# Performance work log

Hardware: AMD Instinct MI355X
Metric: run time of the kernel (lower is better)

Reference implementation:

```python
import jax, jax.numpy as jnp
import numpy as np

D_MODEL = 2048
DOWN = 512
UP = 1024
NUM_HEADS = 16
ROPE_DIM = 64
BS = 16
SEQ = 512
BASE = 10000.0
HEAD_DIM = D_MODEL // NUM_HEADS          # 128 (used only in the softmax scale)
V_HEAD_DIM = UP // NUM_HEADS             # 64


def _linear(x, W, b):
    # torch nn.Linear: y = x @ W.T + b, W shape (out, in)
    return x @ W.T + b


def _rope(x, num_heads, rope_dim):
    # Faithful to source RotaryEmbedding, including the swapped sin/cos caches:
    #   cos_pos = sin(pos*theta), sin_pos = cos(pos*theta)
    bs, L, _ = x.shape
    q = x.reshape(bs, L, num_heads, rope_dim).transpose(0, 2, 1, 3)  # (bs,h,L,d)
    theta = 1.0 / (BASE ** (jnp.arange(0, rope_dim, 2, dtype=jnp.float32) / rope_dim))
    ang = jnp.arange(L, dtype=jnp.float32)[:, None] * theta[None, :]   # (L, d/2)
    cos_pos = jnp.repeat(jnp.sin(ang), 2, axis=-1)  # (L, d) -- source quirk
    sin_pos = jnp.repeat(jnp.cos(ang), 2, axis=-1)
    q2 = jnp.stack([-q[..., 1::2], q[..., ::2]], axis=-1).reshape(bs, num_heads, L, rope_dim)
    return q * cos_pos + q2 * sin_pos


def setup_inputs() -> dict:
    key = jax.random.key(0)
    ks = jax.random.split(key, 18)
    s = 0.02
    d = {
        "h": jax.random.normal(ks[0], (BS, SEQ, D_MODEL), jnp.float32),
        "W_down_kv": jax.random.normal(ks[1], (DOWN, D_MODEL), jnp.float32) * s,
        "b_down_kv": jnp.zeros((DOWN,), jnp.float32),
        "W_up_k": jax.random.normal(ks[2], (UP, DOWN), jnp.float32) * s,
        "b_up_k": jnp.zeros((UP,), jnp.float32),
        "W_up_v": jax.random.normal(ks[3], (UP, DOWN), jnp.float32) * s,
        "b_up_v": jnp.zeros((UP,), jnp.float32),
        "W_down_q": jax.random.normal(ks[4], (DOWN, D_MODEL), jnp.float32) * s,
        "b_down_q": jnp.zeros((DOWN,), jnp.float32),
        "W_up_q": jax.random.normal(ks[5], (UP, DOWN), jnp.float32) * s,
        "b_up_q": jnp.zeros((UP,), jnp.float32),
        "W_qr": jax.random.normal(ks[6], (ROPE_DIM * NUM_HEADS, DOWN), jnp.float32) * s,
        "b_qr": jnp.zeros((ROPE_DIM * NUM_HEADS,), jnp.float32),
        "W_kr": jax.random.normal(ks[7], (ROPE_DIM, D_MODEL), jnp.float32) * s,
        "b_kr": jnp.zeros((ROPE_DIM,), jnp.float32),
        "W_fc": jax.random.normal(ks[8], (D_MODEL, NUM_HEADS * V_HEAD_DIM), jnp.float32) * s,
        "b_fc": jnp.zeros((D_MODEL,), jnp.float32),
    }
    return d


def reference(h, W_down_kv, b_down_kv, W_up_k, b_up_k, W_up_v, b_up_v,
              W_down_q, b_down_q, W_up_q, b_up_q, W_qr, b_qr,
              W_kr, b_kr, W_fc, b_fc):
    bs, L, _ = h.shape
    # low-rank KV path
    c_kv = _linear(h, W_down_kv, b_down_kv)             # (bs,L,down)
    k_c = _linear(c_kv, W_up_k, b_up_k)                 # (bs,L,up)
    v_c = _linear(c_kv, W_up_v, b_up_v)                 # (bs,L,up)
    # low-rank Q path
    c_q = _linear(h, W_down_q, b_down_q)                # (bs,L,down)
    q_c = _linear(c_q, W_up_q, b_up_q)                  # (bs,L,up)
    # rope (decoupled) path
    q_r = _rope(_linear(c_q, W_qr, b_qr), NUM_HEADS, ROPE_DIM)  # (bs,H,L,rope)
    k_r = _rope(_linear(h, W_kr, b_kr), 1, ROPE_DIM)            # (bs,1,L,rope)

    q_c = q_c.reshape(bs, L, NUM_HEADS, -1).transpose(0, 2, 1, 3)  # (bs,H,L,64)
    q = jnp.concatenate([q_c, q_r], axis=-1)                        # (bs,H,L,128)
    k_c = k_c.reshape(bs, L, NUM_HEADS, -1).transpose(0, 2, 1, 3)
    k_r = jnp.broadcast_to(k_r, (bs, NUM_HEADS, L, ROPE_DIM))       # shared across heads
    k = jnp.concatenate([k_c, k_r], axis=-1)

    scale = 1.0 / jnp.sqrt(jnp.float32(HEAD_DIM + ROPE_DIM))  # sqrt(192), per source
    scores = jnp.einsum('bhqd,bhkd->bhqk', q, k) * scale
    attn = jax.nn.softmax(scores, axis=-1)  # dropout is identity in eval mode

    v = v_c.reshape(bs, L, NUM_HEADS, V_HEAD_DIM).transpose(0, 2, 1, 3)
    out = jnp.einsum('bhqk,bhkd->bhqd', attn, v)
    out = out.transpose(0, 2, 1, 3).reshape(bs, L, -1)   # (bs,L,H*v_head_dim)
    return _linear(out, W_fc, b_fc)                      # (bs,L,d_model)
```

## Files before the change

kernel.cpp:

```cpp
#include <hip/hip_runtime.h>
#include <hip/hip_bf16.h>

typedef __bf16 bf16x8 __attribute__((ext_vector_type(8)));
typedef float f32x4 __attribute__((ext_vector_type(4)));
using u16 = unsigned short;
using u32 = unsigned int;

__device__ __forceinline__ float bf2f(u16 v) {
    unsigned int u = (unsigned int)v << 16;
    float f; __builtin_memcpy(&f, &u, 4); return f;
}
__device__ __forceinline__ u16 f2bf(float f) {
    unsigned int u; __builtin_memcpy(&u, &f, 4);
    u += 0x7FFFu + ((u >> 16) & 1u);
    return (u16)(u >> 16);
}

struct Cvt9 {
    const float* src[9];
    u16* dst[9];
    int end[9];
};
__global__ __launch_bounds__(256) void cvt_all(Cvt9 d, int total)
{
    int c = blockIdx.x * 256 + threadIdx.x;
    if (c >= total) return;
    int seg = 0;
    while (c >= d.end[seg]) ++seg;
    int local = c - (seg ? d.end[seg - 1] : 0);
    const float* s = d.src[seg] + (size_t)local * 8;
    float4 f0 = *(const float4*)s;
    float4 f1 = *(const float4*)(s + 4);
    u16 tmp[8] = { f2bf(f0.x), f2bf(f0.y), f2bf(f0.z), f2bf(f0.w),
                   f2bf(f1.x), f2bf(f1.y), f2bf(f1.z), f2bf(f1.w) };
    *(uint4*)(d.dst[seg] + (size_t)local * 8) = *(const uint4*)tmp;
}

struct Cpy7 {
    const float* src[7];
    float* dst[7];
    int end[7];
};
__global__ __launch_bounds__(256) void copy_f32(Cpy7 d, int total)
{
    int c = blockIdx.x * 256 + threadIdx.x;
    if (c >= total) return;
    int seg = 0;
    while (c >= d.end[seg]) ++seg;
    int local = c - (seg ? d.end[seg - 1] : 0);
    d.dst[seg][local] = d.src[seg][local];
}

template<bool CF>
__global__ __launch_bounds__(256) void gemm_v3(
    const u16* __restrict__ A0, const u16* __restrict__ B0, void* __restrict__ C0, const float* __restrict__ e0,
    const u16* __restrict__ A1, const u16* __restrict__ B1, void* __restrict__ C1, const float* __restrict__ e1,
    int ysplit, int lda, int ldb, int ldc, int N, int K)
{
    __shared__ __align__(16) u16 As[128 * 32];
    __shared__ __align__(16) u16 Bs[128 * 32];

    const int t = threadIdx.x;
    const int lane = t & 63;
    const int w = t >> 6;
    const int wm = w >> 1, wn = w & 1;
    const int l16 = lane & 15, quad = lane >> 4;
    const int m0 = blockIdx.x * 128;

    const u16* A; const u16* B; void* Cv; const float* bias; int yl;
    if ((int)blockIdx.y < ysplit) { A = A0; B = B0; Cv = C0; bias = e0; yl = blockIdx.y; }
    else                          { A = A1; B = B1; Cv = C1; bias = e1; yl = blockIdx.y - ysplit; }
    const int n0 = yl * 128;

    const int sub  = lane >> 2;
    const int slot = lane & 3;
    const int agc  = slot ^ ((sub >> 1) & 3);
    const int sfr  = (l16 >> 1) & 3;

    f32x4 acc[4][4];
#pragma unroll
    for (int i = 0; i < 4; ++i)
#pragma unroll
        for (int j = 0; j < 4; ++j) acc[i][j] = (f32x4){0.f, 0.f, 0.f, 0.f};

    for (int k0 = 0; k0 < K; k0 += 32) {
        __syncthreads();
#pragma unroll
        for (int c = 0; c < 2; ++c) {
            const int rr = w * 32 + c * 16;
            const u16* ga = A + (size_t)(m0 + rr + sub) * lda + k0 + agc * 8;
            __builtin_amdgcn_global_load_lds(
                (const __attribute__((address_space(1))) u32*)ga,
                (__attribute__((address_space(3))) u32*)&As[rr * 32], 16, 0, 0);
            const u16* gb = B + (size_t)(n0 + rr + sub) * ldb + k0 + agc * 8;
            __builtin_amdgcn_global_load_lds(
                (const __attribute__((address_space(1))) u32*)gb,
                (__attribute__((address_space(3))) u32*)&Bs[rr * 32], 16, 0, 0);
        }
        __syncthreads();

        bf16x8 af[4], bfr[4];
#pragma unroll
        for (int i = 0; i < 4; ++i)
            af[i] = *(const bf16x8*)&As[(wm * 64 + i * 16 + l16) * 32 + (quad ^ sfr) * 8];
#pragma unroll
        for (int j = 0; j < 4; ++j)
            bfr[j] = *(const bf16x8*)&Bs[(wn * 64 + j * 16 + l16) * 32 + (quad ^ sfr) * 8];
#pragma unroll
        for (int i = 0; i < 4; ++i)
#pragma unroll
            for (int j = 0; j < 4; ++j)
                acc[i][j] = __builtin_amdgcn_mfma_f32_16x16x32_bf16(af[i], bfr[j], acc[i][j], 0, 0, 0);
    }

#pragma unroll
    for (int j = 0; j < 4; ++j) {
        int col = n0 + wn * 64 + j * 16 + l16;
        if (col >= N) continue;
        float bv = bias[col];
#pragma unroll
        for (int i = 0; i < 4; ++i) {
#pragma unroll
            for (int r = 0; r < 4; ++r) {
                int row = m0 + wm * 64 + i * 16 + quad * 4 + r;
                float v = acc[i][j][r] + bv;
                if (CF) ((float*)Cv)[(size_t)row * ldc + col] = v;
                else    ((u16*)Cv)[(size_t)row * ldc + col] = f2bf(v);
            }
        }
    }
}

__global__ void rope_inplace(u16* __restrict__ buf, int ld, int col0, int ppr, int total)
{
    int idx = blockIdx.x * 256 + threadIdx.x;
    if (idx >= total) return;
    int row = idx / ppr;
    int pi  = idx - row * ppr;
    int grp = pi >> 5;
    int i   = pi & 31;
    int pos = row & 511;
    float theta = __expf(-(float)i * 0.2878231366242558f);
    float ang = (float)pos * theta;
    float s = sinf(ang), c = cosf(ang);
    size_t base = (size_t)row * ld + col0 + grp * 64 + 2 * i;
    float x0 = bf2f(buf[base]);
    float x1 = bf2f(buf[base + 1]);
    buf[base]     = f2bf(x0 * s - x1 * c);
    buf[base + 1] = f2bf(x1 * s + x0 * c);
}

__global__ __launch_bounds__(256) void attn_kernel(
    const u16* __restrict__ q_src,
    const u16* __restrict__ kv_src,
    const u16* __restrict__ kr_src,
    u16* __restrict__ o_dst, int ldo)
{
    __shared__ __align__(16) u16 Qs[64 * 136];
    __shared__ __align__(16) u16 Ks[64 * 136];
    __shared__ __align__(16) u16 Vt[64 * 72];
    __shared__ __align__(16) u16 Ps[64 * 72];

    const int t = threadIdx.x;
    const int lane = t & 63;
    const int w = t >> 6;
    const int l16 = lane & 15, quad = lane >> 4;
    const int qt = blockIdx.x;
    const int h  = blockIdx.y;
    const int b  = blockIdx.z;
    const int qrow0 = b * 512 + qt * 64;

#pragma unroll
    for (int p = 0; p < 4; ++p) {
        int ch = t + 256 * p;
        int r = ch >> 4;
        int col = (ch & 15) * 8;
        const u16* src = (col < 64)
            ? q_src + (size_t)(qrow0 + r) * 2048 + h * 64 + col
            : q_src + (size_t)(qrow0 + r) * 2048 + 1024 + h * 64 + (col - 64);
        *(uint4*)&Qs[r * 136 + col] = *(const uint4*)src;
    }

    float m_run[4], l_run[4];
    f32x4 o[4];
#pragma unroll
    for (int r = 0; r < 4; ++r) { m_run[r] = -1e30f; l_run[r] = 0.f; }
#pragma unroll
    for (int n = 0; n < 4; ++n) o[n] = (f32x4){0.f, 0.f, 0.f, 0.f};

    const float scale = 0.07216878364870323f;

    for (int kt = 0; kt < 8; ++kt) {
        __syncthreads();
        const int krow0 = b * 512 + kt * 64;
#pragma unroll
        for (int p = 0; p < 4; ++p) {
            int ch = t + 256 * p;
            int r = ch >> 4;
            int col = (ch & 15) * 8;
            const u16* src = (col < 64)
                ? kv_src + (size_t)(krow0 + r) * 2048 + h * 64 + col
                : kr_src + (size_t)(krow0 + r) * 1088 + 1024 + (col - 64);
            *(uint4*)&Ks[r * 136 + col] = *(const uint4*)src;
        }
#pragma unroll
        for (int p = 0; p < 2; ++p) {
            int ch = t + 256 * p;
            int r = ch >> 3;
            int v0 = (ch & 7) * 8;
            uint4 vv = *(const uint4*)(kv_src + (size_t)(krow0 + r) * 2048 + 1024 + h * 64 + v0);
            u16 tmp[8];
            __builtin_memcpy(tmp, &vv, 16);
#pragma unroll
            for (int j2 = 0; j2 < 8; ++j2)
                Vt[(v0 + j2) * 72 + r] = tmp[j2];
        }
        __syncthreads();

        f32x4 s[4];
#pragma unroll
        for (int n = 0; n < 4; ++n) s[n] = (f32x4){0.f, 0.f, 0.f, 0.f};
#pragma unroll
        for (int ks = 0; ks < 4; ++ks) {
            bf16x8 aq = *(const bf16x8*)&Qs[(w * 16 + l16) * 136 + ks * 32 + quad * 8];
#pragma unroll
            for (int n = 0; n < 4; ++n) {
                bf16x8 bk = *(const bf16x8*)&Ks[(n * 16 + l16) * 136 + ks * 32 + quad * 8];
                s[n] = __builtin_amdgcn_mfma_f32_16x16x32_bf16(aq, bk, s[n], 0, 0, 0);
            }
        }

        float mx[4], alpha[4], rs[4];
#pragma unroll
        for (int r = 0; r < 4; ++r) {
#pragma unroll
            for (int n = 0; n < 4; ++n) s[n][r] *= scale;
            mx[r] = fmaxf(fmaxf(s[0][r], s[1][r]), fmaxf(s[2][r], s[3][r]));
        }
#pragma unroll
        for (int d = 1; d < 16; d <<= 1)
#pragma unroll
            for (int r = 0; r < 4; ++r)
                mx[r] = fmaxf(mx[r], __shfl_xor(mx[r], d));
#pragma unroll
        for (int r = 0; r < 4; ++r) {
            float mnew = fmaxf(m_run[r], mx[r]);
            alpha[r] = __expf(m_run[r] - mnew);
            m_run[r] = mnew;
            rs[r] = 0.f;
#pragma unroll
            for (int n = 0; n < 4; ++n) {
                float pv = __expf(s[n][r] - mnew);
                s[n][r] = pv;
                rs[r] += pv;
            }
        }
#pragma unroll
        for (int d = 1; d < 16; d <<= 1)
#pragma unroll
            for (int r = 0; r < 4; ++r)
                rs[r] += __shfl_xor(rs[r], d);
#pragma unroll
        for (int r = 0; r < 4; ++r) {
            l_run[r] = l_run[r] * alpha[r] + rs[r];
#pragma unroll
            for (int n = 0; n < 4; ++n) o[n][r] *= alpha[r];
        }

#pragma unroll
        for (int n = 0; n < 4; ++n)
#pragma unroll
            for (int r = 0; r < 4; ++r)
                Ps[(w * 16 + quad * 4 + r) * 72 + n * 16 + l16] = f2bf(s[n][r]);
        __syncthreads();

#pragma unroll
        for (int kk = 0; kk < 2; ++kk) {
            bf16x8 ap = *(const bf16x8*)&Ps[(w * 16 + l16) * 72 + kk * 32 + quad * 8];
#pragma unroll
            for (int n = 0; n < 4; ++n) {
                bf16x8 bv = *(const bf16x8*)&Vt[(n * 16 + l16) * 72 + kk * 32 + quad * 8];
                o[n] = __builtin_amdgcn_mfma_f32_16x16x32_bf16(ap, bv, o[n], 0, 0, 0);
            }
        }
    }

#pragma unroll
    for (int n = 0; n < 4; ++n) {
#pragma unroll
        for (int r = 0; r < 4; ++r) {
            int row = qrow0 + w * 16 + quad * 4 + r;
            int col = h * 64 + n * 16 + l16;
            o_dst[(size_t)row * ldo + col] = f2bf(o[n][r] / l_run[r]);
        }
    }
}

extern "C" void kernel_launch(void* const* d_in, const int* in_sizes, int n_in,
                              void* d_out, int out_size, void* d_ws, size_t ws_size,
                              hipStream_t stream)
{
    const float* h    = (const float*)d_in[0];
    const float* Wdkv = (const float*)d_in[1];
    const float* bdkv = (const float*)d_in[2];
    const float* Wuk  = (const float*)d_in[3];
    const float* buk  = (const float*)d_in[4];
    const float* Wuv  = (const float*)d_in[5];
    const float* buv  = (const float*)d_in[6];
    const float* Wdq  = (const float*)d_in[7];
    const float* bdq  = (const float*)d_in[8];
    const float* Wuq  = (const float*)d_in[9];
    const float* buq  = (const float*)d_in[10];
    const float* Wqr  = (const float*)d_in[11];
    const float* bqr  = (const float*)d_in[12];
    const float* Wkr  = (const float*)d_in[13];
    const float* bkr  = (const float*)d_in[14];
    const float* Wfc  = (const float*)d_in[15];
    const float* bfc  = (const float*)d_in[16];

    char* ws = (char*)d_ws;
    u16* out1   = (u16*)ws;
    u16* hbf    = (u16*)(ws + 17825792);
    u16* out2a  = hbf;
    u16* out2b  = (u16*)(ws + 51380224);
    u16* w1     = (u16*)(ws + 84934656);
    u16* w2a    = (u16*)(ws + 89653248);
    u16* w2b    = (u16*)(ws + 91750400);
    u16* wfc    = (u16*)(ws + 93847552);
    float* bias_s1 = (float*)(ws + 98041856);
    float* bias_2  = (float*)(ws + 98046208);

    Cvt9 cd;
    const float* srcs[9] = { h, Wdkv, Wdq, Wkr, Wuk, Wuv, Wuq, Wqr, Wfc };
    u16* dsts[9] = { hbf, w1, w1 + 512 * 2048, w1 + 1024 * 2048,
                     w2a, w2a + 1024 * 512, w2b, w2b + 1024 * 512, wfc };
    int cnts[9] = { 2097152, 131072, 131072, 16384, 65536, 65536, 65536, 65536, 262144 };
    int acc2 = 0;
    for (int i = 0; i < 9; ++i) { cd.src[i] = srcs[i]; cd.dst[i] = dsts[i]; acc2 += cnts[i]; cd.end[i] = acc2; }
    cvt_all<<<(acc2 + 255) / 256, 256, 0, stream>>>(cd, acc2);
    hipMemsetAsync(w1 + 1088 * 2048, 0, 64 * 2048 * sizeof(u16), stream);

    Cpy7 bc;
    const float* bs[7] = { bdkv, bdq, bkr, buk, buv, buq, bqr };
    float* bd[7] = { bias_s1, bias_s1 + 512, bias_s1 + 1024,
                     bias_2, bias_2 + 1024, bias_2 + 2048, bias_2 + 3072 };
    int bn[7] = { 512, 512, 64, 1024, 1024, 1024, 1024 };
    int bacc = 0;
    for (int i = 0; i < 7; ++i) { bc.src[i] = bs[i]; bc.dst[i] = bd[i]; bacc += bn[i]; bc.end[i] = bacc; }
    copy_f32<<<(bacc + 255) / 256, 256, 0, stream>>>(bc, bacc);

    gemm_v3<false><<<dim3(64, 9), 256, 0, stream>>>(
        hbf, w1, out1, bias_s1,
        hbf, w1, out1, bias_s1, 9, 2048, 2048, 1088, 1088, 2048);
    rope_inplace<<<1024, 256, 0, stream>>>(out1, 1088, 1024, 32, 8192 * 32);

    gemm_v3<false><<<dim3(64, 32), 256, 0, stream>>>(
        out1,       w2a, out2a, bias_2,
        out1 + 512, w2b, out2b, bias_2 + 2048, 16, 1088, 512, 2048, 2048, 512);
    rope_inplace<<<16384, 256, 0, stream>>>(out2b, 2048, 1024, 512, 8192 * 512);

    attn_kernel<<<dim3(8, 16, 16), 256, 0, stream>>>(out2b, out2a, out1, out1, 1088);

    gemm_v3<true><<<dim3(64, 16), 256, 0, stream>>>(
        out1, wfc, d_out, bfc,
        out1, wfc, d_out, bfc, 16, 1088, 1024, 2048, 2048, 1024);
}
```

Measured before the change: 476.6 us.

## Keep Q fragments in registers, swizzle P/V LDS layouts, drop barrier

Q fragments now load straight from global memory into registers once per block, so the Q shared-memory tile and its repeated LDS reads go away. The P and transposed V tiles in LDS use rotated column swizzles meant to cut bank conflicts on the scattered writes and vector reads. The barrier between writing P and reading it is removed, relying on each wave reading only its own 16 rows of P. The swizzle arithmetic adds index math, and correctness depends on the rotations matching between writer and reader.

```diff
diff --git a/kernel.cpp b/kernel.cpp
--- a/kernel.cpp
+++ b/kernel.cpp
@@ -156,7 +156,6 @@
     const u16* __restrict__ kr_src,
     u16* __restrict__ o_dst, int ldo)
 {
-    __shared__ __align__(16) u16 Qs[64 * 136];
     __shared__ __align__(16) u16 Ks[64 * 136];
     __shared__ __align__(16) u16 Vt[64 * 72];
     __shared__ __align__(16) u16 Ps[64 * 72];
@@ -170,15 +169,16 @@
     const int b  = blockIdx.z;
     const int qrow0 = b * 512 + qt * 64;
 
-#pragma unroll
-    for (int p = 0; p < 4; ++p) {
-        int ch = t + 256 * p;
-        int r = ch >> 4;
-        int col = (ch & 15) * 8;
-        const u16* src = (col < 64)
-            ? q_src + (size_t)(qrow0 + r) * 2048 + h * 64 + col
-            : q_src + (size_t)(qrow0 + r) * 2048 + 1024 + h * 64 + (col - 64);
-        *(uint4*)&Qs[r * 136 + col] = *(const uint4*)src;
+    bf16x8 aq[4];
+    {
+        const u16* qrow = q_src + (size_t)(qrow0 + w * 16 + l16) * 2048;
+#pragma unroll
+        for (int ks = 0; ks < 4; ++ks) {
+            int col = ks * 32 + quad * 8;
+            const u16* src = (col < 64) ? qrow + h * 64 + col
+                                        : qrow + 1024 + h * 64 + (col - 64);
+            aq[ks] = *(const bf16x8*)src;
+        }
     }
 
     float m_run[4], l_run[4];
@@ -189,6 +189,8 @@
     for (int n = 0; n < 4; ++n) o[n] = (f32x4){0.f, 0.f, 0.f, 0.f};
 
     const float scale = 0.07216878364870323f;
+    const int Rp = (64 - (quad << 4)) & 48;
+    const int Rr = (64 - ((l16 >> 2) << 4)) & 48;
 
     for (int kt = 0; kt < 8; ++kt) {
         __syncthreads();
@@ -211,9 +213,10 @@
             uint4 vv = *(const uint4*)(kv_src + (size_t)(krow0 + r) * 2048 + 1024 + h * 64 + v0);
             u16 tmp[8];
             __builtin_memcpy(tmp, &vv, 16);
+            int rot = (r + v0) & 63;
 #pragma unroll
             for (int j2 = 0; j2 < 8; ++j2)
-                Vt[(v0 + j2) * 72 + r] = tmp[j2];
+                Vt[(v0 + j2) * 72 + rot] = tmp[j2];
         }
         __syncthreads();
 
@@ -222,11 +225,10 @@
         for (int n = 0; n < 4; ++n) s[n] = (f32x4){0.f, 0.f, 0.f, 0.f};
 #pragma unroll
         for (int ks = 0; ks < 4; ++ks) {
-            bf16x8 aq = *(const bf16x8*)&Qs[(w * 16 + l16) * 136 + ks * 32 + quad * 8];
 #pragma unroll
             for (int n = 0; n < 4; ++n) {
                 bf16x8 bk = *(const bf16x8*)&Ks[(n * 16 + l16) * 136 + ks * 32 + quad * 8];
-                s[n] = __builtin_amdgcn_mfma_f32_16x16x32_bf16(aq, bk, s[n], 0, 0, 0);
+                s[n] = __builtin_amdgcn_mfma_f32_16x16x32_bf16(aq[ks], bk, s[n], 0, 0, 0);
             }
         }
 
@@ -268,18 +270,20 @@
         }
 
 #pragma unroll
-        for (int n = 0; n < 4; ++n)
+        for (int n = 0; n < 4; ++n) {
+            int pc = (n * 16 + l16 + Rp) & 63;
 #pragma unroll
             for (int r = 0; r < 4; ++r)
-                Ps[(w * 16 + quad * 4 + r) * 72 + n * 16 + l16] = f2bf(s[n][r]);
-        __syncthreads();
+                Ps[(w * 16 + quad * 4 + r) * 72 + pc] = f2bf(s[n][r]);
+        }
 
 #pragma unroll
         for (int kk = 0; kk < 2; ++kk) {
-            bf16x8 ap = *(const bf16x8*)&Ps[(w * 16 + l16) * 72 + kk * 32 + quad * 8];
+            bf16x8 ap = *(const bf16x8*)&Ps[(w * 16 + l16) * 72 + ((kk * 32 + quad * 8 + Rr) & 63)];
 #pragma unroll
             for (int n = 0; n < 4; ++n) {
-                bf16x8 bv = *(const bf16x8*)&Vt[(n * 16 + l16) * 72 + kk * 32 + quad * 8];
+                bf16x8 bv = *(const bf16x8*)&Vt[(n * 16 + l16) * 72
+                              + ((kk * 32 + quad * 8 + n * 16 + (l16 & 8)) & 63)];
                 o[n] = __builtin_amdgcn_mfma_f32_16x16x32_bf16(ap, bv, o[n], 0, 0, 0);
             }
         }
```

Result: faster. 454.2 us (-4.7%).
